# Kernel optimization log

Hardware: AMD Instinct MI355X
Metric: run time of the kernel (lower is better)

## Reference

```python
import jax, jax.numpy as jnp
import numpy as np

D_MODEL = 1024
D_STATE = 16
D_CONV = 4
EXPAND = 2
D_INNER = EXPAND * D_MODEL          # 2048
DT_RANK = (D_MODEL + 15) // 16      # 64
B, L = 4, 2048


def setup_inputs() -> dict:
    key = jax.random.key(0)
    ks = jax.random.split(key, 10)
    s = 0.02
    x = jax.random.normal(ks[0], (B, L, D_MODEL), dtype=jnp.float32)
    # weights stored (in, out) so y = x @ W
    W_in = jax.random.normal(ks[1], (D_MODEL, 2 * D_INNER), dtype=jnp.float32) * s
    conv_w = jax.random.normal(ks[2], (D_INNER, D_CONV), dtype=jnp.float32) * 0.2
    conv_b = jnp.zeros((D_INNER,), dtype=jnp.float32)
    W_xproj = jax.random.normal(ks[3], (D_INNER, DT_RANK + 2 * D_STATE), dtype=jnp.float32) * s
    W_dt = jax.random.normal(ks[4], (DT_RANK, D_INNER), dtype=jnp.float32) * s
    b_dt = jax.random.uniform(ks[5], (D_INNER,), dtype=jnp.float32, minval=-4.0, maxval=-2.0)
    # S4D real init: A = -exp(A_log), A_log = log(1..d_state)
    A_log = jnp.log(jnp.broadcast_to(jnp.arange(1, D_STATE + 1, dtype=jnp.float32), (D_INNER, D_STATE)))
    Dp = jnp.ones((D_INNER,), dtype=jnp.float32)
    W_out = jax.random.normal(ks[6], (D_INNER, D_MODEL), dtype=jnp.float32) * s
    return {"x": x, "W_in": W_in, "conv_w": conv_w, "conv_b": conv_b,
            "W_xproj": W_xproj, "W_dt": W_dt, "b_dt": b_dt,
            "A_log": A_log, "Dp": Dp, "W_out": W_out}


def _causal_depthwise_conv(u, conv_w, conv_b):
    # u: (B, L, D_INNER); depthwise causal conv, kernel D_CONV
    uc = jnp.transpose(u, (0, 2, 1))                      # (B, D, L)
    k = conv_w[:, None, :]                                # (D, 1, K)
    y = jax.lax.conv_general_dilated(
        uc, k, window_strides=(1,), padding=[(D_CONV - 1, 0)],
        feature_group_count=D_INNER,
        dimension_numbers=('NCH', 'OIH', 'NCH'))
    y = y + conv_b[None, :, None]
    return jnp.transpose(y, (0, 2, 1))                    # (B, L, D)


def _selective_scan(u, delta, A, Bm, Cm, Dp):
    # u, delta: (B, L, d); A: (d, n); Bm, Cm: (B, L, n)
    def step(h, inp):
        u_t, dt_t, B_t, C_t = inp                         # (B,d),(B,d),(B,n),(B,n)
        dA = jnp.exp(dt_t[..., None] * A)                 # (B, d, n)
        h = h * dA + (dt_t * u_t)[..., None] * B_t[:, None, :]
        y = jnp.einsum('bdn,bn->bd', h, C_t)
        return h, y

    h0 = jnp.zeros((u.shape[0], u.shape[2], A.shape[1]), dtype=u.dtype)
    xs = (jnp.swapaxes(u, 0, 1), jnp.swapaxes(delta, 0, 1),
          jnp.swapaxes(Bm, 0, 1), jnp.swapaxes(Cm, 0, 1))
    _, ys = jax.lax.scan(step, h0, xs)
    y = jnp.swapaxes(ys, 0, 1)                            # (B, L, d)
    return y + u * Dp


def reference(x, W_in, conv_w, conv_b, W_xproj, W_dt, b_dt, A_log, Dp, W_out):
    xz = x @ W_in                                         # (B, L, 2*D_INNER)
    u, z = jnp.split(xz, 2, axis=-1)
    u = jax.nn.silu(_causal_depthwise_conv(u, conv_w, conv_b))
    proj = u @ W_xproj                                    # (B, L, DT_RANK + 2*D_STATE)
    dt_r = proj[..., :DT_RANK]
    Bm = proj[..., DT_RANK:DT_RANK + D_STATE]
    Cm = proj[..., DT_RANK + D_STATE:]
    delta = jax.nn.softplus(dt_r @ W_dt + b_dt)           # (B, L, D_INNER)
    A = -jnp.exp(A_log)                                   # (D_INNER, D_STATE)
    y = _selective_scan(u, delta, A, Bm, Cm, Dp)
    y = y * jax.nn.silu(z)
    return y @ W_out
```

## Files before the change

kernel.cpp:

```cpp
#include <hip/hip_runtime.h>
#include <hip/hip_bf16.h>
#include <math.h>

#define MTOK   8192
#define LSEQ   2048
#define NBATCH 4
#define DMODEL 1024
#define DINNER 2048
#define DSTATE 16
#define DTRANK 64
#define NXZ    4096
#define CHUNK  64
#define NCH    32
#define NPROJ  (MTOK * 96)
#define SPLITK 8

typedef _Float16 f16;
using f16x8 = __attribute__((ext_vector_type(8))) _Float16;
using f16x4 = __attribute__((ext_vector_type(4))) _Float16;
using f32x4 = __attribute__((ext_vector_type(4))) float;

__device__ __forceinline__ float silu_f(float x) { return x / (1.f + __expf(-x)); }

__device__ __forceinline__ void gload_lds16(const void* g, void* l) {
    __builtin_amdgcn_global_load_lds(
        (const __attribute__((address_space(1))) void*)g,
        (__attribute__((address_space(3))) void*)l, 16, 0, 0);
}

__global__ __launch_bounds__(256)
void cvt_f2h(const float* __restrict__ in, f16* __restrict__ out, int n4)
{
    const int i = blockIdx.x * 256 + threadIdx.x;
    if (i >= n4) return;
    const float4 v = ((const float4*)in)[i];
    f16x4 o;
    o[0] = (f16)v.x; o[1] = (f16)v.y; o[2] = (f16)v.z; o[3] = (f16)v.w;
    ((f16x4*)out)[i] = o;
}

__global__ __launch_bounds__(256)
void tcvt(const float* __restrict__ in, f16* __restrict__ out, int R, int C)
{
    __shared__ float t[32][33];
    const int c0 = blockIdx.x * 32, r0 = blockIdx.y * 32;
    const int tx = threadIdx.x & 31, ty = threadIdx.x >> 5;
    #pragma unroll
    for (int j = 0; j < 4; ++j)
        t[ty + 8 * j][tx] = in[(size_t)(r0 + ty + 8 * j) * C + c0 + tx];
    __syncthreads();
    #pragma unroll
    for (int j = 0; j < 4; ++j)
        out[(size_t)(c0 + ty + 8 * j) * R + r0 + tx] = (f16)t[tx][ty + 8 * j];
}

__global__ __launch_bounds__(512, 1)
void hgemm256p(const f16* __restrict__ A, int lda,
               const f16* __restrict__ Bt, int ldb,
               f16* __restrict__ C, int ldc,
               int K, f16* __restrict__ C2, int splitcol)
{
    __shared__ __align__(16) f16 SA[2][16384];
    __shared__ __align__(16) f16 SB[2][16384];

    const int tid  = threadIdx.x;
    const int lane = tid & 63, w = tid >> 6;
    const int wr = w >> 2, wc = w & 3;
    const int row0 = blockIdx.x * 256;
    int col0 = blockIdx.y * 256;

    const int frow = lane & 15;
    const int nt = K / 64;

    auto issue_half = [&](int q) {
        const int t = q >> 2, j = q & 3, buf = t & 1, k0 = t * 64;
        const bool isA = (j >= 2);
        const int hh = j & 1;
        const f16* base = isA ? (A  + (size_t)(row0 + hh * 128) * lda + k0)
                              : (Bt + (size_t)(col0 + hh * 128) * ldb + k0);
        const int ld = isA ? lda : ldb;
        f16* dst = (isA ? &SA[buf][0] : &SB[buf][0]) + hh * 8192;
        #pragma unroll
        for (int r2 = 0; r2 < 2; ++r2) {
            const int ch = r2 * 512 + tid;
            const int grow  = ch >> 3;
            const int gunit = (ch & 7) ^ (grow & 7);
            gload_lds16(base + (size_t)grow * ld + gunit * 8, dst + ch * 8);
        }
    };

    int next = 0;
    for (; next < 6 && next < 4 * nt; ++next) issue_half(next);
    asm volatile("s_waitcnt vmcnt(4)" ::: "memory");
    asm volatile("s_barrier" ::: "memory");

    f32x4 acc[8][4] = {};

    for (int t = 0; t < nt; ++t) {
        const int buf = t & 1;
        const char* Ab = (const char*)&SA[buf][0];
        const char* Bb = (const char*)&SB[buf][0];
        f16x8 bf[4][2];
        #pragma unroll
        for (int p = 0; p < 4; ++p) {
            f16x8 af[2][2];
            if (p == 0) {
                #pragma unroll
                for (int n = 0; n < 4; ++n)
                    #pragma unroll
                    for (int ks = 0; ks < 2; ++ks) {
                        const int R = wc * 64 + n * 16 + frow;
                        const int off = R * 128 +
                            ((ks * 64 + (lane >> 4) * 16) ^ ((R & 7) << 4));
                        bf[n][ks] = *(const f16x8*)(Bb + off);
                    }
            }
            #pragma unroll
            for (int i = 0; i < 2; ++i)
                #pragma unroll
                for (int ks = 0; ks < 2; ++ks) {
                    const int R = wr * 128 + (2 * p + i) * 16 + frow;
                    const int off = R * 128 +
                        ((ks * 64 + (lane >> 4) * 16) ^ ((R & 7) << 4));
                    af[i][ks] = *(const f16x8*)(Ab + off);
                }
            if (next < 4 * nt) issue_half(next++);
            asm volatile("s_barrier" ::: "memory");
            asm volatile("s_waitcnt lgkmcnt(0)" ::: "memory");
            __builtin_amdgcn_sched_barrier(0);
            __builtin_amdgcn_s_setprio(1);
            #pragma unroll
            for (int i = 0; i < 2; ++i)
                #pragma unroll
                for (int n = 0; n < 4; ++n)
                    #pragma unroll
                    for (int ks = 0; ks < 2; ++ks)
                        acc[2 * p + i][n] = __builtin_amdgcn_mfma_f32_16x16x32_f16(
                            af[i][ks], bf[n][ks], acc[2 * p + i][n], 0, 0, 0);
            __builtin_amdgcn_s_setprio(0);
            if (p == 3 && t + 1 < nt) {
                if (next >= 4 * t + 10) asm volatile("s_waitcnt vmcnt(4)" ::: "memory");
                else                    asm volatile("s_waitcnt vmcnt(0)" ::: "memory");
            }
            asm volatile("s_barrier" ::: "memory");
        }
    }

    f16* Cw = C;
    if (C2 != nullptr && col0 >= splitcol) { Cw = C2; col0 -= splitcol; }

    const int rbase = row0 + wr * 128 + (lane >> 4) * 4;
    const int cbase = col0 + wc * 64 + (lane & 15);
    #pragma unroll
    for (int m = 0; m < 8; ++m) {
        #pragma unroll
        for (int n = 0; n < 4; ++n) {
            const int col = cbase + n * 16;
            #pragma unroll
            for (int r = 0; r < 4; ++r)
                Cw[(size_t)(rbase + m * 16 + r) * ldc + col] = (f16)acc[m][n][r];
        }
    }
}

template<int EPI, typename OUT_T>
__global__ __launch_bounds__(256)
void hgemm128(const f16* __restrict__ A, int lda,
              const f16* __restrict__ Bt, int ldb,
              OUT_T* __restrict__ C, int ldc,
              int K, const float* __restrict__ bias,
              OUT_T* __restrict__ C2, int splitcol)
{
    __shared__ __align__(16) f16 As[2][128 * 32];
    __shared__ __align__(16) f16 Bs[2][128 * 32];

    const int tid  = threadIdx.x;
    const int lane = tid & 63, wave = tid >> 6;
    const int wr = wave >> 1, wc = wave & 1;
    const int row0 = blockIdx.x * 128;
    int col0 = blockIdx.y * 128;

    const int lrow = lane >> 2;
    const int lcol = ((lane & 3) ^ ((lane >> 3) & 3)) * 8;
    const f16* Agw = A  + (size_t)(row0 + wave * 32 + lrow) * lda + lcol;
    const f16* Bgw = Bt + (size_t)(col0 + wave * 32 + lrow) * ldb + lcol;
    const int ldsbase = (wave * 32) * 32;

    const int frow = lane & 15;
    const int fk   = (((lane >> 4) ^ ((frow >> 1) & 3))) * 8;
    const int nt = K / 32;

    f32x4 acc[4][4] = {};

    #pragma unroll
    for (int r = 0; r < 2; ++r) {
        gload_lds16(Agw + (size_t)r * 16 * lda, &As[0][ldsbase + r * 16 * 32]);
        gload_lds16(Bgw + (size_t)r * 16 * ldb, &Bs[0][ldsbase + r * 16 * 32]);
    }

    int cur = 0;
    for (int kt = 0; kt < nt; ++kt) {
        __syncthreads();
        if (kt + 1 < nt) {
            const int k0 = (kt + 1) * 32;
            #pragma unroll
            for (int r = 0; r < 2; ++r) {
                gload_lds16(Agw + (size_t)r * 16 * lda + k0, &As[cur ^ 1][ldsbase + r * 16 * 32]);
                gload_lds16(Bgw + (size_t)r * 16 * ldb + k0, &Bs[cur ^ 1][ldsbase + r * 16 * 32]);
            }
        }
        f16x8 af[4], bf[4];
        #pragma unroll
        for (int m = 0; m < 4; ++m)
            af[m] = *(const f16x8*)&As[cur][(wr * 64 + m * 16 + frow) * 32 + fk];
        #pragma unroll
        for (int n = 0; n < 4; ++n)
            bf[n] = *(const f16x8*)&Bs[cur][(wc * 64 + n * 16 + frow) * 32 + fk];
        #pragma unroll
        for (int m = 0; m < 4; ++m)
            #pragma unroll
            for (int n = 0; n < 4; ++n)
                acc[m][n] = __builtin_amdgcn_mfma_f32_16x16x32_f16(af[m], bf[n], acc[m][n], 0, 0, 0);
        cur ^= 1;
    }

    OUT_T* Cw = C;
    if (C2 != nullptr && col0 >= splitcol) { Cw = C2; col0 -= splitcol; }

    const int rbase = row0 + wr * 64 + (lane >> 4) * 4;
    const int cbase = col0 + wc * 64 + (lane & 15);
    #pragma unroll
    for (int m = 0; m < 4; ++m) {
        #pragma unroll
        for (int n = 0; n < 4; ++n) {
            const int col = cbase + n * 16;
            #pragma unroll
            for (int r = 0; r < 4; ++r) {
                const int row = rbase + m * 16 + r;
                float tv = acc[m][n][r];
                if (EPI == 1) {
                    tv += bias[col];
                    tv = (tv > 20.f) ? tv : __logf(1.f + __expf(tv));
                }
                Cw[(size_t)row * ldc + col] = (OUT_T)tv;
            }
        }
    }
}

__global__ __launch_bounds__(256)
void hgemm_n96(const f16* __restrict__ A,
               const f16* __restrict__ Bt,
               float* __restrict__ part)
{
    __shared__ __align__(16) f16 As[128][40];
    __shared__ __align__(16) f16 Bs[96][40];

    const int tid = threadIdx.x, lane = tid & 63, wave = tid >> 6;
    const int row0 = blockIdx.x * 128;
    const int sk = blockIdx.y;
    const int kbase = sk * (DINNER / SPLITK);

    const int srow = tid >> 1, skoff = (tid & 1) * 16;
    const f16* Ag = A  + (size_t)(row0 + srow) * DINNER + kbase + skoff;
    const f16* Bg = Bt + (size_t)srow * DINNER + kbase + skoff;

    const int frow = lane & 15, fk = (lane >> 4) * 8;

    f32x4 acc[2][6] = {};

    for (int kk = 0; kk < DINNER / SPLITK; kk += 32) {
        const f16x8 a0 = *(const f16x8*)(Ag + kk);
        const f16x8 a1 = *(const f16x8*)(Ag + kk + 8);
        f16x8 b0 = {}, b1 = {};
        if (tid < 192) { b0 = *(const f16x8*)(Bg + kk); b1 = *(const f16x8*)(Bg + kk + 8); }
        __syncthreads();
        *(f16x8*)&As[srow][skoff]     = a0;
        *(f16x8*)&As[srow][skoff + 8] = a1;
        if (tid < 192) {
            *(f16x8*)&Bs[srow][skoff]     = b0;
            *(f16x8*)&Bs[srow][skoff + 8] = b1;
        }
        __syncthreads();

        f16x8 af[2], bf[6];
        #pragma unroll
        for (int m = 0; m < 2; ++m)
            af[m] = *(const f16x8*)&As[wave * 32 + m * 16 + frow][fk];
        #pragma unroll
        for (int n = 0; n < 6; ++n)
            bf[n] = *(const f16x8*)&Bs[n * 16 + frow][fk];
        #pragma unroll
        for (int m = 0; m < 2; ++m)
            #pragma unroll
            for (int n = 0; n < 6; ++n)
                acc[m][n] = __builtin_amdgcn_mfma_f32_16x16x32_f16(af[m], bf[n], acc[m][n], 0, 0, 0);
    }

    #pragma unroll
    for (int m = 0; m < 2; ++m)
        #pragma unroll
        for (int n = 0; n < 6; ++n) {
            const int col = n * 16 + (lane & 15);
            #pragma unroll
            for (int r = 0; r < 4; ++r) {
                const int row = row0 + wave * 32 + m * 16 + (lane >> 4) * 4 + r;
                part[((size_t)sk * MTOK + row) * 96 + col] = acc[m][n][r];
            }
        }
}

__global__ __launch_bounds__(256)
void reduce3(const float* __restrict__ part, float* __restrict__ proj,
             f16* __restrict__ projh)
{
    const int e = blockIdx.x * 256 + threadIdx.x;
    float s = 0.f;
    #pragma unroll
    for (int i = 0; i < SPLITK; ++i) s += part[(size_t)i * NPROJ + e];
    proj[e]  = s;
    projh[e] = (f16)s;
}

__global__ __launch_bounds__(256)
void conv_silu_kernel(const f16* __restrict__ uph,
                      const float* __restrict__ cw, const float* __restrict__ cb,
                      f16* __restrict__ uh)
{
    const int mt  = blockIdx.x;
    const int ml0 = mt * 8;
    const int l0  = ml0 & (LSEQ - 1);
    const int d   = threadIdx.x * 8;

    float w[8][4];
    #pragma unroll
    for (int c = 0; c < 8; ++c) {
        const float4 wv = *(const float4*)(cw + (size_t)(d + c) * 4);
        w[c][0] = wv.x; w[c][1] = wv.y; w[c][2] = wv.z; w[c][3] = wv.w;
    }
    float bias[8];
    {
        const float4 b0 = *(const float4*)(cb + d);
        const float4 b1 = *(const float4*)(cb + d + 4);
        bias[0] = b0.x; bias[1] = b0.y; bias[2] = b0.z; bias[3] = b0.w;
        bias[4] = b1.x; bias[5] = b1.y; bias[6] = b1.z; bias[7] = b1.w;
    }

    f16x8 r[11];
    if (l0 != 0) {
        #pragma unroll
        for (int i = 0; i < 11; ++i)
            r[i] = *(const f16x8*)(uph + (size_t)(ml0 - 3 + i) * DINNER + d);
    } else {
        r[0] = f16x8{}; r[1] = f16x8{}; r[2] = f16x8{};
        #pragma unroll
        for (int i = 3; i < 11; ++i)
            r[i] = *(const f16x8*)(uph + (size_t)(ml0 - 3 + i) * DINNER + d);
    }

    #pragma unroll
    for (int i = 0; i < 8; ++i) {
        f16x8 o;
        #pragma unroll
        for (int c = 0; c < 8; ++c) {
            float a = bias[c];
            #pragma unroll
            for (int j = 0; j < 4; ++j)
                a = fmaf((float)r[i + j][c], w[c][j], a);
            o[c] = (f16)silu_f(a);
        }
        *(f16x8*)(uh + (size_t)(ml0 + i) * DINNER + d) = o;
    }
}

__device__ __forceinline__ bool load_A(const float* __restrict__ A_log, int d,
                                       float* Av)
{
    #pragma unroll
    for (int n = 0; n < DSTATE; ++n)
        Av[n] = -__expf(A_log[(size_t)d * DSTATE + n]);
    bool p = true;
    #pragma unroll
    for (int n = 1; n < DSTATE; ++n) {
        const float r = Av[n] / Av[0];
        if (fabsf(r - (float)(n + 1)) > 1e-3f) p = false;
    }
    return p;
}

__global__ __launch_bounds__(256)
void scan_pass1(const f16* __restrict__ uh,
                const f16* __restrict__ deltah,
                const float* __restrict__ proj,
                const float* __restrict__ A_log,
                float* __restrict__ Sbuf, float* __restrict__ sumdt)
{
    const int d = blockIdx.x * 256 + threadIdx.x;
    const int c = blockIdx.y;
    const int b = blockIdx.z;

    float Av[DSTATE];
    const bool pw = load_A(A_log, d, Av);
    const float Av0 = Av[0];

    const float* projb = proj + ((size_t)b * LSEQ + (size_t)c * CHUNK) * 96 + 64;

    float S[DSTATE];
    #pragma unroll
    for (int n = 0; n < DSTATE; ++n) S[n] = 0.f;
    float sdt = 0.f;

    const size_t tok0 = (size_t)b * LSEQ + (size_t)c * CHUNK;
    if (pw) {
        for (int l = 0; l < CHUNK; ++l) {
            const float* pr = projb + (size_t)l * 96;
            const float dt = (float)deltah[(tok0 + l) * DINNER + d];
            const float uu = (float)uh[(tok0 + l) * DINNER + d];
            sdt += dt;
            const float du = dt * uu;
            const float p1 = __expf(dt * Av0);
            const float p2 = p1 * p1;
            const float p3 = p2 * p1;
            const float p4 = p2 * p2;
            float m = 1.f;
            #pragma unroll
            for (int g = 0; g < 4; ++g) {
                const f32x4 bb = *(const f32x4*)(pr + g * 4);
                S[g*4+0] = fmaf(S[g*4+0], m * p1, du * bb[0]);
                S[g*4+1] = fmaf(S[g*4+1], m * p2, du * bb[1]);
                S[g*4+2] = fmaf(S[g*4+2], m * p3, du * bb[2]);
                S[g*4+3] = fmaf(S[g*4+3], m * p4, du * bb[3]);
                m *= p4;
            }
        }
    } else {
        for (int l = 0; l < CHUNK; ++l) {
            const float* pr = projb + (size_t)l * 96;
            const float dt = (float)deltah[(tok0 + l) * DINNER + d];
            const float uu = (float)uh[(tok0 + l) * DINNER + d];
            sdt += dt;
            const float du = dt * uu;
            #pragma unroll
            for (int n = 0; n < DSTATE; ++n)
                S[n] = fmaf(S[n], __expf(dt * Av[n]), du * pr[n]);
        }
    }

    const size_t base = (size_t)b * NCH + c;
    #pragma unroll
    for (int n = 0; n < DSTATE; ++n)
        Sbuf[(base * DSTATE + n) * DINNER + d] = S[n];
    sumdt[base * DINNER + d] = sdt;
}

__global__ __launch_bounds__(256)
void scan_pass2(const float* __restrict__ A_log,
                const float* __restrict__ sumdt,
                float* __restrict__ Sbuf)
{
    const int d = blockIdx.x * 256 + threadIdx.x;
    const int b = blockIdx.y;

    float Av[DSTATE];
    const bool pw = load_A(A_log, d, Av);
    const float Av0 = Av[0];

    float h[DSTATE];
    #pragma unroll
    for (int n = 0; n < DSTATE; ++n) h[n] = 0.f;

    for (int c = 0; c < NCH; ++c) {
        const size_t base = (size_t)b * NCH + c;
        const float sdt = sumdt[base * DINNER + d];
        if (pw) {
            const float p1 = __expf(sdt * Av0);
            const float p2 = p1 * p1;
            const float p3 = p2 * p1;
            const float p4 = p2 * p2;
            float m = 1.f;
            #pragma unroll
            for (int g = 0; g < 4; ++g) {
                const float pj[4] = {p1, p2, p3, p4};
                #pragma unroll
                for (int j = 0; j < 4; ++j) {
                    const int n = g * 4 + j;
                    const size_t idx = (base * DSTATE + n) * DINNER + d;
                    const float tmp = Sbuf[idx];
                    Sbuf[idx] = h[n];
                    h[n] = fmaf(h[n], m * pj[j], tmp);
                }
                m *= p4;
            }
        } else {
            #pragma unroll
            for (int n = 0; n < DSTATE; ++n) {
                const size_t idx = (base * DSTATE + n) * DINNER + d;
                const float tmp = Sbuf[idx];
                Sbuf[idx] = h[n];
                h[n] = fmaf(h[n], __expf(sdt * Av[n]), tmp);
            }
        }
    }
}

__global__ __launch_bounds__(256)
void scan_pass3(const f16* __restrict__ uh,
                const f16* __restrict__ deltah,
                const f16* __restrict__ zh,
                const float* __restrict__ proj,
                const float* __restrict__ A_log,
                const float* __restrict__ Dp,
                const float* __restrict__ Sbuf,
                f16* __restrict__ ygh)
{
    const int d = blockIdx.x * 256 + threadIdx.x;
    const int c = blockIdx.y;
    const int b = blockIdx.z;

    float Av[DSTATE];
    const bool pw = load_A(A_log, d, Av);
    const float Av0 = Av[0];

    float h[DSTATE];
    const size_t base = (size_t)b * NCH + c;
    #pragma unroll
    for (int n = 0; n < DSTATE; ++n)
        h[n] = Sbuf[(base * DSTATE + n) * DINNER + d];

    const float Dval = Dp[d];
    const float* projb = proj + ((size_t)b * LSEQ + (size_t)c * CHUNK) * 96 + 64;

    const size_t tok0 = (size_t)b * LSEQ + (size_t)c * CHUNK;
    for (int l = 0; l < CHUNK; ++l) {
        const float* pr = projb + (size_t)l * 96;
        const size_t tok = tok0 + l;
        const float dt = (float)deltah[tok * DINNER + d];
        const float uu = (float)uh[tok * DINNER + d];
        const float zz = (float)zh[tok * DINNER + d];
        const float du = dt * uu;
        float y = 0.f;
        if (pw) {
            const float p1 = __expf(dt * Av0);
            const float p2 = p1 * p1;
            const float p3 = p2 * p1;
            const float p4 = p2 * p2;
            float m = 1.f;
            #pragma unroll
            for (int g = 0; g < 4; ++g) {
                const f32x4 bb = *(const f32x4*)(pr + g * 4);
                const f32x4 cc = *(const f32x4*)(pr + 16 + g * 4);
                h[g*4+0] = fmaf(h[g*4+0], m * p1, du * bb[0]);
                h[g*4+1] = fmaf(h[g*4+1], m * p2, du * bb[1]);
                h[g*4+2] = fmaf(h[g*4+2], m * p3, du * bb[2]);
                h[g*4+3] = fmaf(h[g*4+3], m * p4, du * bb[3]);
                y = fmaf(h[g*4+0], cc[0], y);
                y = fmaf(h[g*4+1], cc[1], y);
                y = fmaf(h[g*4+2], cc[2], y);
                y = fmaf(h[g*4+3], cc[3], y);
                m *= p4;
            }
        } else {
            #pragma unroll
            for (int n = 0; n < DSTATE; ++n) {
                h[n] = fmaf(h[n], __expf(dt * Av[n]), du * pr[n]);
                y = fmaf(h[n], pr[16 + n], y);
            }
        }
        const float yt = fmaf(uu, Dval, y);
        ygh[tok * DINNER + d] = (f16)(yt * silu_f(zz));
    }
}

extern "C" void kernel_launch(void* const* d_in, const int* in_sizes, int n_in,
                              void* d_out, int out_size, void* d_ws, size_t ws_size,
                              hipStream_t stream)
{
    const float* x     = (const float*)d_in[0];
    const float* W_in  = (const float*)d_in[1];
    const float* cw    = (const float*)d_in[2];
    const float* cb    = (const float*)d_in[3];
    const float* W_xp  = (const float*)d_in[4];
    const float* W_dt  = (const float*)d_in[5];
    const float* b_dt  = (const float*)d_in[6];
    const float* A_log = (const float*)d_in[7];
    const float* Dp    = (const float*)d_in[8];
    const float* W_out = (const float*)d_in[9];
    float* out = (float*)d_out;

    float* updelta = (float*)d_ws;
    f16*   zh      = (f16*)(updelta + (size_t)MTOK * DINNER);
    f16*   uh      = zh + (size_t)MTOK * DINNER;
    float* proj    = (float*)(uh + (size_t)MTOK * DINNER);
    f16*   projh   = (f16*)(proj + NPROJ);
    float* Sbuf    = (float*)(projh + NPROJ);
    float* sumdt   = Sbuf + (size_t)NBATCH * NCH * DSTATE * DINNER;
    f16*   WxpT    = (f16*)(sumdt + (size_t)NBATCH * NCH * DINNER);
    f16*   WdtT    = WxpT + (size_t)96 * DINNER;
    f16*   WoutT   = WdtT + (size_t)DINNER * DTRANK;
    f16*   big     = WoutT + (size_t)DMODEL * DINNER;
    f16*   WinT    = big;
    float* part3   = (float*)(big + (size_t)NXZ * DMODEL);
    f16*   ygh     = big;
    f16*   xh      = uh;
    f16*   uph     = (f16*)updelta;
    f16*   deltah  = (f16*)updelta;

    cvt_f2h<<<(MTOK * DMODEL / 4 + 255) / 256, 256, 0, stream>>>(x, xh, MTOK * DMODEL / 4);
    tcvt<<<dim3(NXZ / 32, DMODEL / 32), 256, 0, stream>>>(W_in, WinT, DMODEL, NXZ);

    hgemm256p<<<dim3(32, 16), 512, 0, stream>>>(
        xh, DMODEL, WinT, DMODEL, uph, DINNER, DMODEL, zh, DINNER);

    conv_silu_kernel<<<MTOK / 8, 256, 0, stream>>>(uph, cw, cb, uh);

    tcvt<<<dim3(96 / 32, DINNER / 32), 256, 0, stream>>>(W_xp, WxpT, DINNER, 96);
    hgemm_n96<<<dim3(64, SPLITK), 256, 0, stream>>>(uh, WxpT, part3);
    reduce3<<<NPROJ / 256, 256, 0, stream>>>(part3, proj, projh);

    tcvt<<<dim3(DINNER / 32, DTRANK / 32), 256, 0, stream>>>(W_dt, WdtT, DTRANK, DINNER);
    hgemm128<1, f16><<<dim3(64, 16), 256, 0, stream>>>(
        projh, 96, WdtT, DTRANK, deltah, DINNER, DTRANK, b_dt, nullptr, 0);

    scan_pass1<<<dim3(DINNER / 256, NCH, NBATCH), 256, 0, stream>>>(
        uh, deltah, proj, A_log, Sbuf, sumdt);
    scan_pass2<<<dim3(DINNER / 256, NBATCH), 256, 0, stream>>>(A_log, sumdt, Sbuf);
    scan_pass3<<<dim3(DINNER / 256, NCH, NBATCH), 256, 0, stream>>>(
        uh, deltah, zh, proj, A_log, Dp, Sbuf, ygh);

    tcvt<<<dim3(DMODEL / 32, DINNER / 32), 256, 0, stream>>>(W_out, WoutT, DINNER, DMODEL);
    hgemm128<0, float><<<dim3(64, 8), 256, 0, stream>>>(
        ygh, DINNER, WoutT, DINNER, out, DMODEL, DINNER, nullptr, nullptr, 0);
}
```

Baseline: 317.2 us.

## Store chunk states in fp16, parallelize scan pass2 over states, halve split-K

The inter-chunk state buffer is now stored in fp16 rather than fp32, halving its traffic across all three scan passes. Pass2 is re-parallelized so each thread carries a single (d, n) state rather than all 16, which raises the block count from 32 to 512. The x_proj GEMM split-K factor drops from 8 to 4, reducing partial-sum reduction work. In exchange, chunk-boundary states lose precision in fp16, pass2 recomputes an exp per state instead of using the power trick, and pass2 reads sumdt once per state instead of once per thread.

```diff
diff --git a/kernel.cpp b/kernel.cpp
--- a/kernel.cpp
+++ b/kernel.cpp
@@ -13,7 +13,7 @@
 #define CHUNK  64
 #define NCH    32
 #define NPROJ  (MTOK * 96)
-#define SPLITK 8
+#define SPLITK 4
 
 typedef _Float16 f16;
 using f16x8 = __attribute__((ext_vector_type(8))) _Float16;
@@ -393,7 +393,7 @@
                 const f16* __restrict__ deltah,
                 const float* __restrict__ proj,
                 const float* __restrict__ A_log,
-                float* __restrict__ Sbuf, float* __restrict__ sumdt)
+                f16* __restrict__ Sbufh, float* __restrict__ sumdt)
 {
     const int d = blockIdx.x * 256 + threadIdx.x;
     const int c = blockIdx.y;
@@ -449,57 +449,29 @@
     const size_t base = (size_t)b * NCH + c;
     #pragma unroll
     for (int n = 0; n < DSTATE; ++n)
-        Sbuf[(base * DSTATE + n) * DINNER + d] = S[n];
+        Sbufh[(base * DSTATE + n) * DINNER + d] = (f16)S[n];
     sumdt[base * DINNER + d] = sdt;
 }
 
 __global__ __launch_bounds__(256)
 void scan_pass2(const float* __restrict__ A_log,
                 const float* __restrict__ sumdt,
-                float* __restrict__ Sbuf)
-{
-    const int d = blockIdx.x * 256 + threadIdx.x;
-    const int b = blockIdx.y;
-
-    float Av[DSTATE];
-    const bool pw = load_A(A_log, d, Av);
-    const float Av0 = Av[0];
-
-    float h[DSTATE];
-    #pragma unroll
-    for (int n = 0; n < DSTATE; ++n) h[n] = 0.f;
-
+                f16* __restrict__ Sbufh)
+{
+    const int d = blockIdx.x * 64 + (threadIdx.x & 63);
+    const int n = blockIdx.y * 4 + (threadIdx.x >> 6);
+    const int b = blockIdx.z;
+
+    const float Avn = -__expf(A_log[(size_t)d * DSTATE + n]);
+
+    float h = 0.f;
     for (int c = 0; c < NCH; ++c) {
         const size_t base = (size_t)b * NCH + c;
         const float sdt = sumdt[base * DINNER + d];
-        if (pw) {
-            const float p1 = __expf(sdt * Av0);
-            const float p2 = p1 * p1;
-            const float p3 = p2 * p1;
-            const float p4 = p2 * p2;
-            float m = 1.f;
-            #pragma unroll
-            for (int g = 0; g < 4; ++g) {
-                const float pj[4] = {p1, p2, p3, p4};
-                #pragma unroll
-                for (int j = 0; j < 4; ++j) {
-                    const int n = g * 4 + j;
-                    const size_t idx = (base * DSTATE + n) * DINNER + d;
-                    const float tmp = Sbuf[idx];
-                    Sbuf[idx] = h[n];
-                    h[n] = fmaf(h[n], m * pj[j], tmp);
-                }
-                m *= p4;
-            }
-        } else {
-            #pragma unroll
-            for (int n = 0; n < DSTATE; ++n) {
-                const size_t idx = (base * DSTATE + n) * DINNER + d;
-                const float tmp = Sbuf[idx];
-                Sbuf[idx] = h[n];
-                h[n] = fmaf(h[n], __expf(sdt * Av[n]), tmp);
-            }
-        }
+        const size_t idx = (base * DSTATE + n) * DINNER + d;
+        const float tmp = (float)Sbufh[idx];
+        Sbufh[idx] = (f16)h;
+        h = fmaf(h, __expf(sdt * Avn), tmp);
     }
 }
 
@@ -510,7 +482,7 @@
                 const float* __restrict__ proj,
                 const float* __restrict__ A_log,
                 const float* __restrict__ Dp,
-                const float* __restrict__ Sbuf,
+                const f16* __restrict__ Sbufh,
                 f16* __restrict__ ygh)
 {
     const int d = blockIdx.x * 256 + threadIdx.x;
@@ -525,7 +497,7 @@
     const size_t base = (size_t)b * NCH + c;
     #pragma unroll
     for (int n = 0; n < DSTATE; ++n)
-        h[n] = Sbuf[(base * DSTATE + n) * DINNER + d];
+        h[n] = (float)Sbufh[(base * DSTATE + n) * DINNER + d];
 
     const float Dval = Dp[d];
     const float* projb = proj + ((size_t)b * LSEQ + (size_t)c * CHUNK) * 96 + 64;
@@ -592,8 +564,8 @@
     f16*   uh      = zh + (size_t)MTOK * DINNER;
     float* proj    = (float*)(uh + (size_t)MTOK * DINNER);
     f16*   projh   = (f16*)(proj + NPROJ);
-    float* Sbuf    = (float*)(projh + NPROJ);
-    float* sumdt   = Sbuf + (size_t)NBATCH * NCH * DSTATE * DINNER;
+    f16*   Sbufh   = (f16*)(projh + NPROJ);
+    float* sumdt   = (float*)(Sbufh + (size_t)NBATCH * NCH * DSTATE * DINNER * 2);
     f16*   WxpT    = (f16*)(sumdt + (size_t)NBATCH * NCH * DINNER);
     f16*   WdtT    = WxpT + (size_t)96 * DINNER;
     f16*   WoutT   = WdtT + (size_t)DINNER * DTRANK;
@@ -622,10 +594,11 @@
         projh, 96, WdtT, DTRANK, deltah, DINNER, DTRANK, b_dt, nullptr, 0);
 
     scan_pass1<<<dim3(DINNER / 256, NCH, NBATCH), 256, 0, stream>>>(
-        uh, deltah, proj, A_log, Sbuf, sumdt);
-    scan_pass2<<<dim3(DINNER / 256, NBATCH), 256, 0, stream>>>(A_log, sumdt, Sbuf);
+        uh, deltah, proj, A_log, Sbufh, sumdt);
+    scan_pass2<<<dim3(DINNER / 64, DSTATE / 4, NBATCH), 256, 0, stream>>>(
+        A_log, sumdt, Sbufh);
     scan_pass3<<<dim3(DINNER / 256, NCH, NBATCH), 256, 0, stream>>>(
-        uh, deltah, zh, proj, A_log, Dp, Sbuf, ygh);
+        uh, deltah, zh, proj, A_log, Dp, Sbufh, ygh);
 
     tcvt<<<dim3(DMODEL / 32, DINNER / 32), 256, 0, stream>>>(W_out, WoutT, DINNER, DMODEL);
     hgemm128<0, float><<<dim3(64, 8), 256, 0, stream>>>(
```

New measurement: 296.9 us. 1.07x faster.
